# Kernel optimization log

Measured on AMD Instinct MI355X. Metric: run time of the kernel, lower is better.

The kernel has to match this reference:

```python
import jax, jax.numpy as jnp
import numpy as np

STAGE = 100  # number of weight bins


def _bin_reconstruct(w, affine):
    # Faithful vectorization of the 100-iter binning loop: element in bin i
    # (half-open interval) gets scaled by affine[i]; the max element falls
    # outside every bin (w < wmin + stage*range/stage fails) and is zeroed.
    flat = w.reshape(-1)
    wmin, wmax = flat.min(), flat.max()
    idx = jnp.floor((flat - wmin) / (wmax - wmin) * STAGE).astype(jnp.int32)
    mask = (idx < STAGE).astype(flat.dtype)  # mask is detached in torch (non-diff anyway)
    scale = affine[jnp.clip(idx, 0, STAGE - 1)]
    return flat * scale * mask


def _kl_vs_laplace(new_flat, lap):
    # F.kl_div(log_softmax(w), softmax(lap), reduction='none').mean()
    logq = jax.nn.log_softmax(new_flat)
    p = jax.nn.softmax(lap)
    return (p * (jnp.log(p) - logq)).mean()


def _adder2d(x, w, stride, padding, groups=1):
    # AdderNet conv: out = -sum_k |patch_k - w_k| (no bias)
    O, Cg, kh, kw = w.shape
    patches = jax.lax.conv_general_dilated_patches(
        x, (kh, kw), (stride, stride), [(padding, padding), (padding, padding)])
    B, _, Hp, Wp = patches.shape  # channel dim ordered (C, kh, kw), C-major
    if groups == 1:
        p = patches.reshape(B, 1, Cg * kh * kw, Hp, Wp)
        wf = w.reshape(1, O, Cg * kh * kw, 1, 1)
    else:  # depthwise: groups == C_in, Cg == 1, O == C_in
        p = patches.reshape(B, O, kh * kw, Hp, Wp)
        wf = w.reshape(1, O, kh * kw, 1, 1)
    return -jnp.abs(p - wf).sum(axis=2)  # [B, O, Hp, Wp]


def _bn_train(x, g, b, eps=1e-5):
    # BatchNorm2d in training mode (batch statistics, biased variance)
    m = x.mean(axis=(0, 2, 3), keepdims=True)
    v = ((x - m) ** 2).mean(axis=(0, 2, 3), keepdims=True)
    return (x - m) * jax.lax.rsqrt(v + eps) * g.reshape(1, -1, 1, 1) + b.reshape(1, -1, 1, 1)


def _forward(x, sw_ds, sw_c1, sw_c2, sw_c3, a_ds, a_c1, a_c2, a_c3, peg_w,
             g1, b1, g2, b2, g3, b3, gds, bds, lap_ds, lap_c1, lap_c2, lap_c3):
    kl = jnp.float32(0.0)
    f_ds = _bin_reconstruct(sw_ds, a_ds)
    kl = kl + _kl_vs_laplace(f_ds, lap_ds)
    f_c1 = _bin_reconstruct(sw_c1, a_c1)
    kl = kl + _kl_vs_laplace(f_c1, lap_c1)
    residual = jax.nn.relu(_bn_train(_adder2d(x, f_ds.reshape(sw_ds.shape), 1, 0), gds, bds))
    h = _adder2d(x, f_c1.reshape(sw_c1.shape), 1, 0)
    h = _adder2d(h, peg_w, 1, 1, groups=peg_w.shape[0])  # PEG depthwise 3x3
    h = jax.nn.relu(_bn_train(h, g1, b1))
    f_c2 = _bin_reconstruct(sw_c2, a_c2)
    kl = kl + _kl_vs_laplace(f_c2, lap_c2)
    h = _adder2d(h, f_c2.reshape(sw_c2.shape), 1, 1)
    h = jax.nn.relu(_bn_train(h, g2, b2))
    f_c3 = _bin_reconstruct(sw_c3, a_c3)
    kl = kl + _kl_vs_laplace(f_c3, lap_c3)
    h = _adder2d(h, f_c3.reshape(sw_c3.shape), 1, 0)
    h = _bn_train(h, g3, b3)  # bn3 gamma zero-initialized
    return jax.nn.relu(h + residual), kl


def setup_inputs() -> dict:
    key = jax.random.key(0)
    ks = jax.random.split(key, 16)
    inp = {
        'x': jax.random.normal(ks[0], (4, 128, 28, 28), jnp.float32),
        'sw_downsample': jax.random.normal(ks[1], (256, 128, 1, 1), jnp.float32) * 0.05,
        'sw_conv1': jax.random.normal(ks[2], (64, 128, 1, 1), jnp.float32) * 0.05,
        'sw_conv2': jax.random.normal(ks[3], (64, 64, 3, 3), jnp.float32) * 0.05,
        'sw_conv3': jax.random.normal(ks[4], (256, 64, 1, 1), jnp.float32) * 0.05,
        'downsample_affine': jax.random.normal(ks[5], (100,), jnp.float32),
        'conv1_affine': jax.random.normal(ks[6], (100,), jnp.float32),
        'conv2_affine': jax.random.normal(ks[7], (100,), jnp.float32),
        'conv3_affine': jax.random.normal(ks[8], (100,), jnp.float32),
        'peg_w': jax.random.normal(ks[9], (64, 1, 3, 3), jnp.float32) * 0.05,
        'bn1_g': jnp.ones((64,), jnp.float32), 'bn1_b': jnp.zeros((64,), jnp.float32),
        'bn2_g': jnp.ones((64,), jnp.float32), 'bn2_b': jnp.zeros((64,), jnp.float32),
        'bn3_g': jnp.zeros((256,), jnp.float32), 'bn3_b': jnp.zeros((256,), jnp.float32),
        'bnds_g': jnp.ones((256,), jnp.float32), 'bnds_b': jnp.zeros((256,), jnp.float32),
        # Laplace(0, 2) samples, drawn once in setup so the reference is deterministic
        'lap_ds': jax.random.laplace(ks[10], (32768,), jnp.float32) * 2.0,
        'lap_c1': jax.random.laplace(ks[11], (8192,), jnp.float32) * 2.0,
        'lap_c2': jax.random.laplace(ks[12], (36864,), jnp.float32) * 2.0,
        'lap_c3': jax.random.laplace(ks[13], (16384,), jnp.float32) * 2.0,
    }
    return inp


def reference(x, sw_downsample, sw_conv1, sw_conv2, sw_conv3,
              downsample_affine, conv1_affine, conv2_affine, conv3_affine, peg_w,
              bn1_g, bn1_b, bn2_g, bn2_b, bn3_g, bn3_b, bnds_g, bnds_b,
              lap_ds, lap_c1, lap_c2, lap_c3):
    return _forward(x, sw_downsample, sw_conv1, sw_conv2, sw_conv3,
                    downsample_affine, conv1_affine, conv2_affine, conv3_affine, peg_w,
                    bn1_g, bn1_b, bn2_g, bn2_b, bn3_g, bn3_b, bnds_g, bnds_b,
                    lap_ds, lap_c1, lap_c2, lap_c3)
```

## Files before the change

kernel.cpp:

```cpp
#include <hip/hip_runtime.h>
#include <math.h>


#define HW 784
#define NB 4
#define STAGE 100

__device__ __forceinline__ float wredSum(float v){
  for (int o = 32; o > 0; o >>= 1) v += __shfl_down(v, o, 64);
  return v;
}
__device__ __forceinline__ float wredMax(float v){
  for (int o = 32; o > 0; o >>= 1) v = fmaxf(v, __shfl_down(v, o, 64));
  return v;
}
__device__ __forceinline__ float wredMin(float v){
  for (int o = 32; o > 0; o >>= 1) v = fminf(v, __shfl_down(v, o, 64));
  return v;
}
__device__ __forceinline__ double wredSumD(double v){
  for (int o = 32; o > 0; o >>= 1) v += __shfl_down(v, o, 64);
  return v;
}

__device__ float blockMin4(float v){
  __shared__ float shn[4];
  __syncthreads();
  v = wredMin(v);
  if ((threadIdx.x & 63) == 0) shn[threadIdx.x >> 6] = v;
  __syncthreads();
  return fminf(fminf(shn[0], shn[1]), fminf(shn[2], shn[3]));
}
__device__ float blockMax4(float v){
  __shared__ float shx[4];
  __syncthreads();
  v = wredMax(v);
  if ((threadIdx.x & 63) == 0) shx[threadIdx.x >> 6] = v;
  __syncthreads();
  return fmaxf(fmaxf(shx[0], shx[1]), fmaxf(shx[2], shx[3]));
}

__device__ void stats4(float v0, float v1, float v2, float v3,
                       double* sumP, double* sqP, int oc0){
  __shared__ double sred[4][8];
  __syncthreads();
  const int w = threadIdx.x >> 6;
  float vv[4] = {v0, v1, v2, v3};
  #pragma unroll
  for (int i = 0; i < 4; i++){
    double d = (double)vv[i];
    double s = wredSumD(d);
    double q = wredSumD(d * d);
    if ((threadIdx.x & 63) == 0){ sred[w][i] = s; sred[w][4 + i] = q; }
  }
  __syncthreads();
  if (threadIdx.x < 8){
    double tot = sred[0][threadIdx.x] + sred[1][threadIdx.x]
               + sred[2][threadIdx.x] + sred[3][threadIdx.x];
    int i = threadIdx.x & 3;
    if (threadIdx.x < 4) atomicAdd(&sumP[oc0 + i], tot);
    else                 atomicAdd(&sqP[oc0 + i],  tot);
  }
}
__device__ void stats2(float v0, float v1, double* sumP, double* sqP, int oc0){
  __shared__ double sred2[4][4];
  __syncthreads();
  const int w = threadIdx.x >> 6;
  float vv[2] = {v0, v1};
  #pragma unroll
  for (int i = 0; i < 2; i++){
    double d = (double)vv[i];
    double s = wredSumD(d);
    double q = wredSumD(d * d);
    if ((threadIdx.x & 63) == 0){ sred2[w][i] = s; sred2[w][2 + i] = q; }
  }
  __syncthreads();
  if (threadIdx.x < 4){
    double tot = sred2[0][threadIdx.x] + sred2[1][threadIdx.x]
               + sred2[2][threadIdx.x] + sred2[3][threadIdx.x];
    int i = threadIdx.x & 1;
    if (threadIdx.x < 2) atomicAdd(&sumP[oc0 + i], tot);
    else                 atomicAdd(&sqP[oc0 + i],  tot);
  }
}

__device__ void klAccum(float se, float sel, float sef, float sq, double* dst){
  __shared__ double kls[4][4];
  __syncthreads();
  const int w = threadIdx.x >> 6;
  double a0 = wredSumD((double)se);
  double a1 = wredSumD((double)sel);
  double a2 = wredSumD((double)sef);
  double a3 = wredSumD((double)sq);
  if ((threadIdx.x & 63) == 0){
    kls[w][0] = a0; kls[w][1] = a1; kls[w][2] = a2; kls[w][3] = a3;
  }
  __syncthreads();
  if (threadIdx.x < 4){
    double tot = kls[0][threadIdx.x] + kls[1][threadIdx.x]
               + kls[2][threadIdx.x] + kls[3][threadIdx.x];
    atomicAdd(&dst[threadIdx.x], tot);
  }
}

__device__ __forceinline__ float reconv(float vv, float mn, float rng,
                                        const float* saff){
  float q = (vv - mn) / rng * 100.0f;
  int idx = (int)floorf(q);
  float nv = 0.0f;
  if (idx < STAGE){
    int ci = idx < 0 ? 0 : (idx > STAGE - 1 ? STAGE - 1 : idx);
    nv = vv * saff[ci];
  }
  return nv;
}

__device__ __forceinline__ void mmReduce(const float* mmbuf, int tens,
                                         float& mn, float& mx){
  mn = 3.402823466e38f; mx = -3.402823466e38f;
  #pragma unroll
  for (int k = 0; k < 16; k++){
    mn = fminf(mn, mmbuf[tens * 32 + k]);
    mx = fmaxf(mx, mmbuf[tens * 32 + 16 + k]);
  }
}

__global__ __launch_bounds__(256) void minmax_kernel(
    const float* w0, int n0, const float* w1, int n1,
    const float* w2, int n2, const float* w3, int n3,
    float* mmbuf, double* dstat)
{
  if (threadIdx.x < 21) dstat[blockIdx.x * 21 + threadIdx.x] = 0.0;
  const int tens = blockIdx.x >> 4, slot = blockIdx.x & 15;
  const float* w; int n;
  if      (tens == 0){ w = w0; n = n0; }
  else if (tens == 1){ w = w1; n = n1; }
  else if (tens == 2){ w = w2; n = n2; }
  else               { w = w3; n = n3; }
  float mn = 3.402823466e38f, mx = -3.402823466e38f;
  for (int i = slot * 256 + threadIdx.x; i < n; i += 4096){
    float v = w[i];
    mn = fminf(mn, v); mx = fmaxf(mx, v);
  }
  mn = blockMin4(mn); mx = blockMax4(mx);
  if (threadIdx.x == 0){
    mmbuf[tens * 32 + slot]      = mn;
    mmbuf[tens * 32 + 16 + slot] = mx;
  }
}

__global__ __launch_bounds__(256) void front_kernel(
    const float* __restrict__ x,
    const float* __restrict__ w_ds, const float* __restrict__ aff_ds,
    const float* __restrict__ lap_ds,
    const float* __restrict__ w_c1, const float* __restrict__ aff_c1,
    const float* __restrict__ lap_c1,
    const float* __restrict__ w_c2, const float* __restrict__ aff_c2,
    const float* __restrict__ lap_c2, float* __restrict__ f_c2,
    const float* __restrict__ w_c3, const float* __restrict__ aff_c3,
    const float* __restrict__ lap_c3,
    const float* __restrict__ peg_w, const float* __restrict__ mmbuf,
    float* __restrict__ A, float* __restrict__ T2, double* __restrict__ dS)
{
  const int t = threadIdx.x;
  if (blockIdx.x < 512){
    const int a = blockIdx.x;
    const int chunk = a & 3, og = (a >> 2) & 31, b = a >> 7;
    const int oc0 = og * 8;
    __shared__ float saff[STAGE];
    __shared__ float sw[1024];
    if (t < STAGE) saff[t] = aff_ds[t];
    float mn, mx; mmReduce(mmbuf, 0, mn, mx);
    const float rng = mx - mn;
    __syncthreads();
    for (int k = t; k < 1024; k += 256)
      sw[k] = reconv(w_ds[oc0 * 128 + k], mn, rng, saff);
    __syncthreads();

    const int px = chunk * 196 + t;
    float v0=0,v1=0,v2=0,v3=0,v4=0,v5=0,v6=0,v7=0;
    if (t < 196){
      const float* xp = x + (size_t)b * 128 * HW + px;
      float c0=0,c1=0,c2=0,c3=0,c4=0,c5=0,c6=0,c7=0;
      #pragma unroll 4
      for (int c = 0; c < 128; c++){
        float xv = xp[(size_t)c * HW];
        c0 += fabsf(xv - sw[c]);
        c1 += fabsf(xv - sw[128 + c]);
        c2 += fabsf(xv - sw[256 + c]);
        c3 += fabsf(xv - sw[384 + c]);
        c4 += fabsf(xv - sw[512 + c]);
        c5 += fabsf(xv - sw[640 + c]);
        c6 += fabsf(xv - sw[768 + c]);
        c7 += fabsf(xv - sw[896 + c]);
      }
      v0=-c0; v1=-c1; v2=-c2; v3=-c3; v4=-c4; v5=-c5; v6=-c6; v7=-c7;
      float* op = A + ((size_t)(b * 256 + oc0)) * HW + px;
      op[0]=v0; op[HW]=v1; op[2*HW]=v2; op[3*HW]=v3;
      op[4*HW]=v4; op[5*HW]=v5; op[6*HW]=v6; op[7*HW]=v7;
    }
    stats4(v0, v1, v2, v3, dS + 0, dS + 256, oc0);
    stats4(v4, v5, v6, v7, dS + 0, dS + 256, oc0 + 4);

    if (b == 0 && chunk == 0){
      float se = 0, sel = 0, sef = 0, sq = 0;
      for (int k = t; k < 1024; k += 256){
        float l = lap_ds[oc0 * 128 + k];
        float e = expf(l);
        se += e; sel += e * l; sef += e * sw[k];
        sq += expf(sw[k]);
      }
      klAccum(se, sel, sef, sq, dS + 1280 + 0);
    }
  } else if (blockIdx.x < 768){
    const int a = blockIdx.x - 512;
    const int rc = a & 3, og = (a >> 2) & 15, b = a >> 6;
    const int oc0 = og * 4;
    __shared__ float saffc[STAGE];
    __shared__ float swc[512];
    __shared__ float swp[36];
    __shared__ float sT1[4][256];
    if (t < STAGE) saffc[t] = aff_c1[t];
    if (t >= 128 && t < 164) swp[t - 128] = peg_w[oc0 * 9 + (t - 128)];
    float mn, mx; mmReduce(mmbuf, 1, mn, mx);
    const float rng = mx - mn;
    __syncthreads();
    for (int k = t; k < 512; k += 256)
      swc[k] = reconv(w_c1[oc0 * 128 + k], mn, rng, saffc);
    __syncthreads();

    if (t < 252){
      const int rr = t / 28;
      const int col = t - rr * 28;
      const int wr = rc * 7 - 1 + rr;
      float tv0 = 0, tv1 = 0, tv2 = 0, tv3 = 0;
      if (wr >= 0 && wr < 28){
        const float* xp = x + (size_t)b * 128 * HW + wr * 28 + col;
        float c0 = 0, c1 = 0, c2 = 0, c3 = 0;
        #pragma unroll 4
        for (int c = 0; c < 128; c++){
          float xv = xp[(size_t)c * HW];
          c0 += fabsf(xv - swc[c]);
          c1 += fabsf(xv - swc[128 + c]);
          c2 += fabsf(xv - swc[256 + c]);
          c3 += fabsf(xv - swc[384 + c]);
        }
        tv0 = -c0; tv1 = -c1; tv2 = -c2; tv3 = -c3;
      }
      sT1[0][t] = tv0; sT1[1][t] = tv1; sT1[2][t] = tv2; sT1[3][t] = tv3;
    }
    __syncthreads();
    float v0 = 0, v1 = 0, v2 = 0, v3 = 0;
    if (t < 196){
      const int r = t / 28, col = t - r * 28;
      float c0 = 0, c1 = 0, c2 = 0, c3 = 0;
      #pragma unroll
      for (int ky = 0; ky < 3; ky++){
        #pragma unroll
        for (int kx = 0; kx < 3; kx++){
          int cc = col + kx - 1;
          bool ok = (cc >= 0) && (cc < 28);
          int idx = ok ? ((r + ky) * 28 + cc) : 0;
          float p0 = ok ? sT1[0][idx] : 0.0f;
          float p1 = ok ? sT1[1][idx] : 0.0f;
          float p2 = ok ? sT1[2][idx] : 0.0f;
          float p3 = ok ? sT1[3][idx] : 0.0f;
          int wk = ky * 3 + kx;
          c0 += fabsf(p0 - swp[wk]);
          c1 += fabsf(p1 - swp[9 + wk]);
          c2 += fabsf(p2 - swp[18 + wk]);
          c3 += fabsf(p3 - swp[27 + wk]);
        }
      }
      v0 = -c0; v1 = -c1; v2 = -c2; v3 = -c3;
      const int opx = (rc * 7 + r) * 28 + col;
      float* op = T2 + ((size_t)(b * 64 + oc0)) * HW + opx;
      op[0] = v0; op[HW] = v1; op[2 * HW] = v2; op[3 * HW] = v3;
    }
    stats4(v0, v1, v2, v3, dS + 512, dS + 576, oc0);

    if (b == 0 && rc == 0){
      float se = 0, sel = 0, sef = 0, sq = 0;
      for (int k = t; k < 512; k += 256){
        float l = lap_c1[oc0 * 128 + k];
        float e = expf(l);
        se += e; sel += e * l; sef += e * swc[k];
        sq += expf(swc[k]);
      }
      klAccum(se, sel, sef, sq, dS + 1280 + 4);
    }
  } else if (blockIdx.x < 832){
    const int j = blockIdx.x - 768;
    __shared__ float saff2[STAGE];
    if (t < STAGE) saff2[t] = aff_c2[t];
    float mn, mx; mmReduce(mmbuf, 2, mn, mx);
    const float rng = mx - mn;
    __syncthreads();
    float se = 0, sel = 0, sef = 0, sq = 0;
    for (int k = t; k < 576; k += 256){
      float nv = reconv(w_c2[j * 576 + k], mn, rng, saff2);
      f_c2[j * 576 + k] = nv;
      float l = lap_c2[j * 576 + k];
      float e = expf(l);
      se += e; sel += e * l; sef += e * nv; sq += expf(nv);
    }
    klAccum(se, sel, sef, sq, dS + 1280 + 8);
  } else {
    const int j = blockIdx.x - 832;
    __shared__ float saff3[STAGE];
    if (t < STAGE) saff3[t] = aff_c3[t];
    float mn, mx; mmReduce(mmbuf, 3, mn, mx);
    const float rng = mx - mn;
    __syncthreads();
    float se = 0, sel = 0, sef = 0, sq = 0;
    for (int k = t; k < 1024; k += 256){
      float nv = reconv(w_c3[j * 1024 + k], mn, rng, saff3);
      float l = lap_c3[j * 1024 + k];
      float e = expf(l);
      se += e; sel += e * l; sef += e * nv; sq += expf(nv);
    }
    klAccum(se, sel, sef, sq, dS + 1280 + 12);
  }
}

__global__ __launch_bounds__(256) void bnapply_pad_kernel(
    const float* __restrict__ T2, float* __restrict__ T2b,
    const float* __restrict__ g1, const float* __restrict__ b1,
    const double* __restrict__ dS)
{
  const int a = blockIdx.x;
  const int c = a & 63, b = a >> 6;
  __shared__ float ssc, ssb;
  if (threadIdx.x == 0){
    double s  = dS[512 + c] * (1.0 / 3136.0);
    double vr = dS[576 + c] * (1.0 / 3136.0) - s * s;
    float scale = g1[c] * rsqrtf((float)vr + 1e-5f);
    ssc = scale; ssb = b1[c] - (float)s * scale;
  }
  __syncthreads();
  const float sc_ = ssc, bi_ = ssb;
  const float* src = T2 + (size_t)a * HW;
  float* dst = T2b + (size_t)a * 960;
  for (int i = threadIdx.x; i < 960; i += 256){
    int row = i >> 5, col = i & 31;
    float v = 0.0f;
    if (row >= 1 && row <= 28 && col >= 1 && col <= 28)
      v = fmaxf(src[(row - 1) * 28 + (col - 1)] * sc_ + bi_, 0.0f);
    dst[i] = v;
  }
}

__global__ __launch_bounds__(256) void mid3x3_kernel(
    const float* __restrict__ T2b, const float* __restrict__ f_c2,
    float* __restrict__ T3, double* __restrict__ dS)
{
  const int t = threadIdx.x;
  const int a = blockIdx.x;
  const int chunk = a & 3, og = (a >> 2) & 31, b = a >> 7;
  const int oc0 = og * 2;
  const float* __restrict__ wA = f_c2 + oc0 * 576;
  const float* __restrict__ wB = wA + 576;

  float v0 = 0, v1 = 0;
  const int px = chunk * 196 + t;
  if (t < 196){
    const int y = px / 28, xc = px - y * 28;
    const float* base = T2b + (size_t)b * 64 * 960 + y * 32 + xc;
    float c0 = 0, c1 = 0;
    #pragma unroll 2
    for (int c = 0; c < 64; c++){
      const float* p = base + c * 960;
      float t0 = p[0],  t1 = p[1],  t2 = p[2];
      float t3 = p[32], t4 = p[33], t5 = p[34];
      float t6 = p[64], t7 = p[65], t8 = p[66];
      const float* wa = wA + c * 9;
      const float* wb = wB + c * 9;
      c0 += fabsf(t0 - wa[0]) + fabsf(t1 - wa[1]) + fabsf(t2 - wa[2])
          + fabsf(t3 - wa[3]) + fabsf(t4 - wa[4]) + fabsf(t5 - wa[5])
          + fabsf(t6 - wa[6]) + fabsf(t7 - wa[7]) + fabsf(t8 - wa[8]);
      c1 += fabsf(t0 - wb[0]) + fabsf(t1 - wb[1]) + fabsf(t2 - wb[2])
          + fabsf(t3 - wb[3]) + fabsf(t4 - wb[4]) + fabsf(t5 - wb[5])
          + fabsf(t6 - wb[6]) + fabsf(t7 - wb[7]) + fabsf(t8 - wb[8]);
    }
    v0 = -c0; v1 = -c1;
    T3[((size_t)(b * 64 + oc0)) * HW + px]     = v0;
    T3[((size_t)(b * 64 + oc0 + 1)) * HW + px] = v1;
  }
  stats2(v0, v1, dS + 640, dS + 704, oc0);
}

__global__ __launch_bounds__(256) void back_kernel(
    const float* __restrict__ T3, const float* __restrict__ w_c3,
    const float* __restrict__ aff_c3, const float* __restrict__ mmbuf,
    const float* __restrict__ g2, const float* __restrict__ b2,
    float* __restrict__ out, double* __restrict__ dS)
{
  const int t = threadIdx.x;
  const int a = blockIdx.x;
  const int chunk = a & 3, og = (a >> 2) & 63, b = a >> 8;
  const int oc0 = og * 4;
  __shared__ float ssc[64], ssb[64], sw[256], saff[STAGE];
  if (t < 64){
    double s  = dS[640 + t] * (1.0 / 3136.0);
    double vr = dS[704 + t] * (1.0 / 3136.0) - s * s;
    float scale = g2[t] * rsqrtf((float)vr + 1e-5f);
    ssc[t] = scale; ssb[t] = b2[t] - (float)s * scale;
  }
  if (t >= 128 && t < 128 + STAGE) saff[t - 128] = aff_c3[t - 128];
  float mn, mx; mmReduce(mmbuf, 3, mn, mx);
  const float rng = mx - mn;
  __syncthreads();
  sw[t] = reconv(w_c3[oc0 * 64 + t], mn, rng, saff);
  __syncthreads();

  const int px = chunk * 196 + t;
  float v0 = 0, v1 = 0, v2 = 0, v3 = 0;
  if (t < 196){
    const float* bp = T3 + (size_t)b * 64 * HW + px;
    float c0 = 0, c1 = 0, c2 = 0, c3 = 0;
    #pragma unroll 4
    for (int c = 0; c < 64; c++){
      float raw = bp[(size_t)c * HW];
      float vv = fmaxf(raw * ssc[c] + ssb[c], 0.0f);
      c0 += fabsf(vv - sw[c]);
      c1 += fabsf(vv - sw[64 + c]);
      c2 += fabsf(vv - sw[128 + c]);
      c3 += fabsf(vv - sw[192 + c]);
    }
    v0 = -c0; v1 = -c1; v2 = -c2; v3 = -c3;
    float* op = out + ((size_t)(b * 256 + oc0)) * HW + px;
    op[0] = v0; op[HW] = v1; op[2 * HW] = v2; op[3 * HW] = v3;
  }
  stats4(v0, v1, v2, v3, dS + 768, dS + 1024, oc0);
}

__global__ __launch_bounds__(256) void final_kernel(
    float* __restrict__ out, const float* __restrict__ A,
    const float* __restrict__ g3, const float* __restrict__ b3,
    const float* __restrict__ gds, const float* __restrict__ bds,
    const double* __restrict__ dS)
{
  __shared__ float s3c[256], s3b[256], sdc[256], sdb[256];
  const int t = threadIdx.x;
  {
    double s  = dS[768 + t] * (1.0 / 3136.0);
    double vr = dS[1024 + t] * (1.0 / 3136.0) - s * s;
    float scale = g3[t] * rsqrtf((float)vr + 1e-5f);
    s3c[t] = scale; s3b[t] = b3[t] - (float)s * scale;
    s  = dS[t] * (1.0 / 3136.0);
    vr = dS[256 + t] * (1.0 / 3136.0) - s * s;
    scale = gds[t] * rsqrtf((float)vr + 1e-5f);
    sdc[t] = scale; sdb[t] = bds[t] - (float)s * scale;
  }
  __syncthreads();
  #pragma unroll
  for (int k = 0; k < 4; k++){
    int n = blockIdx.x * 1024 + k * 256 + t;
    int c = (n / HW) & 255;
    float h = out[n], aa = A[n];
    float r = fmaxf(aa * sdc[c] + sdb[c], 0.0f);
    out[n] = fmaxf(h * s3c[c] + s3b[c] + r, 0.0f);
  }
  if (blockIdx.x == 0 && t == 0){
    const int ns[4] = {32768, 8192, 36864, 16384};
    float kl = 0.0f;
    #pragma unroll
    for (int q = 0; q < 4; q++){
      double se  = dS[1280 + q * 4];
      double sel = dS[1280 + q * 4 + 1];
      double sef = dS[1280 + q * 4 + 2];
      double sq  = dS[1280 + q * 4 + 3];
      kl += (float)((((sel - sef) / se) - log(se) + log(sq)) / (double)ns[q]);
    }
    out[802816] = kl;
  }
}

extern "C" void kernel_launch(void* const* d_in, const int* in_sizes, int n_in,
                              void* d_out, int out_size, void* d_ws, size_t ws_size,
                              hipStream_t stream)
{
  const float* x      = (const float*)d_in[0];
  const float* sw_ds  = (const float*)d_in[1];
  const float* sw_c1  = (const float*)d_in[2];
  const float* sw_c2  = (const float*)d_in[3];
  const float* sw_c3  = (const float*)d_in[4];
  const float* a_ds   = (const float*)d_in[5];
  const float* a_c1   = (const float*)d_in[6];
  const float* a_c2   = (const float*)d_in[7];
  const float* a_c3   = (const float*)d_in[8];
  const float* peg_w  = (const float*)d_in[9];
  const float* bn1_g  = (const float*)d_in[10];
  const float* bn1_b  = (const float*)d_in[11];
  const float* bn2_g  = (const float*)d_in[12];
  const float* bn2_b  = (const float*)d_in[13];
  const float* bn3_g  = (const float*)d_in[14];
  const float* bn3_b  = (const float*)d_in[15];
  const float* bnds_g = (const float*)d_in[16];
  const float* bnds_b = (const float*)d_in[17];
  const float* lap_ds = (const float*)d_in[18];
  const float* lap_c1 = (const float*)d_in[19];
  const float* lap_c2 = (const float*)d_in[20];
  const float* lap_c3 = (const float*)d_in[21];

  float* ws    = (float*)d_ws;
  float* f_c2  = ws;
  float* mmbuf = ws + 36864;
  double* dstat= (double*)(ws + 37120);
  float* A     = ws + 39808;
  float* T2    = ws + 842624;
  float* T3    = ws + 1043328;
  float* T2b   = ws + 1244032;

  float* out = (float*)d_out;

  minmax_kernel<<<64, 256, 0, stream>>>(
      sw_ds, 32768, sw_c1, 8192, sw_c2, 36864, sw_c3, 16384, mmbuf, dstat);

  front_kernel<<<848, 256, 0, stream>>>(
      x, sw_ds, a_ds, lap_ds, sw_c1, a_c1, lap_c1,
      sw_c2, a_c2, lap_c2, f_c2, sw_c3, a_c3, lap_c3,
      peg_w, mmbuf, A, T2, dstat);

  bnapply_pad_kernel<<<256, 256, 0, stream>>>(T2, T2b, bn1_g, bn1_b, dstat);

  mid3x3_kernel<<<512, 256, 0, stream>>>(T2b, f_c2, T3, dstat);

  back_kernel<<<1024, 256, 0, stream>>>(T3, sw_c3, a_c3, mmbuf,
                                        bn2_g, bn2_b, out, dstat);

  final_kernel<<<784, 256, 0, stream>>>(out, A, bn3_g, bn3_b, bnds_g, bnds_b,
                                        dstat);
}
```

Baseline: 171.8 us.

## Fuse all stages into one persistent cooperative kernel with grid syncs

Replaces the six separate kernel launches with a single cooperative kernel of 512 blocks. Stages are separated by grid.sync(), and the work of each former kernel is remapped onto the fixed block count, with some blocks running two units. This removes per-launch overhead and inter-kernel gaps. In exchange it adds grid-wide barrier costs, imbalanced per-block work in the front stage, and a shared-memory footprint that is the union of every stage, which may limit occupancy.

```diff
diff --git a/kernel.cpp b/kernel.cpp
--- a/kernel.cpp
+++ b/kernel.cpp
@@ -1,15 +1,22 @@
 #include <hip/hip_runtime.h>
+#include <hip/hip_cooperative_groups.h>
 #include <math.h>
 
+
+namespace cg = cooperative_groups;
 
 #define HW 784
 #define NB 4
 #define STAGE 100
 
-__device__ __forceinline__ float wredSum(float v){
-  for (int o = 32; o > 0; o >>= 1) v += __shfl_down(v, o, 64);
-  return v;
-}
+struct Params {
+  const float *x, *w_ds, *a_ds, *lap_ds, *w_c1, *a_c1, *lap_c1;
+  const float *w_c2, *a_c2, *lap_c2, *w_c3, *a_c3, *lap_c3;
+  const float *peg_w, *g1, *b1, *g2, *b2, *g3, *b3, *gds, *bds;
+  float *f_c2, *mmbuf, *A, *T2, *T2b, *T3, *out;
+  double *dstat;
+};
+
 __device__ __forceinline__ float wredMax(float v){
   for (int o = 32; o > 0; o >>= 1) v = fmaxf(v, __shfl_down(v, o, 64));
   return v;
@@ -22,7 +29,6 @@
   for (int o = 32; o > 0; o >>= 1) v += __shfl_down(v, o, 64);
   return v;
 }
-
 __device__ float blockMin4(float v){
   __shared__ float shn[4];
   __syncthreads();
@@ -39,7 +45,6 @@
   __syncthreads();
   return fmaxf(fmaxf(shx[0], shx[1]), fmaxf(shx[2], shx[3]));
 }
-
 __device__ void stats4(float v0, float v1, float v2, float v3,
                        double* sumP, double* sqP, int oc0){
   __shared__ double sred[4][8];
@@ -83,7 +88,6 @@
     else                 atomicAdd(&sqP[oc0 + i],  tot);
   }
 }
-
 __device__ void klAccum(float se, float sel, float sef, float sq, double* dst){
   __shared__ double kls[4][4];
   __syncthreads();
@@ -102,7 +106,6 @@
     atomicAdd(&dst[threadIdx.x], tot);
   }
 }
-
 __device__ __forceinline__ float reconv(float vv, float mn, float rng,
                                         const float* saff){
   float q = (vv - mn) / rng * 100.0f;
@@ -114,7 +117,6 @@
   }
   return nv;
 }
-
 __device__ __forceinline__ void mmReduce(const float* mmbuf, int tens,
                                          float& mn, float& mx){
   mn = 3.402823466e38f; mx = -3.402823466e38f;
@@ -125,223 +127,190 @@
   }
 }
 
-__global__ __launch_bounds__(256) void minmax_kernel(
-    const float* w0, int n0, const float* w1, int n1,
-    const float* w2, int n2, const float* w3, int n3,
-    float* mmbuf, double* dstat)
-{
-  if (threadIdx.x < 21) dstat[blockIdx.x * 21 + threadIdx.x] = 0.0;
-  const int tens = blockIdx.x >> 4, slot = blockIdx.x & 15;
-  const float* w; int n;
-  if      (tens == 0){ w = w0; n = n0; }
-  else if (tens == 1){ w = w1; n = n1; }
-  else if (tens == 2){ w = w2; n = n2; }
-  else               { w = w3; n = n3; }
-  float mn = 3.402823466e38f, mx = -3.402823466e38f;
-  for (int i = slot * 256 + threadIdx.x; i < n; i += 4096){
-    float v = w[i];
-    mn = fminf(mn, v); mx = fmaxf(mx, v);
-  }
-  mn = blockMin4(mn); mx = blockMax4(mx);
-  if (threadIdx.x == 0){
-    mmbuf[tens * 32 + slot]      = mn;
-    mmbuf[tens * 32 + 16 + slot] = mx;
-  }
-}
-
-__global__ __launch_bounds__(256) void front_kernel(
-    const float* __restrict__ x,
-    const float* __restrict__ w_ds, const float* __restrict__ aff_ds,
-    const float* __restrict__ lap_ds,
-    const float* __restrict__ w_c1, const float* __restrict__ aff_c1,
-    const float* __restrict__ lap_c1,
-    const float* __restrict__ w_c2, const float* __restrict__ aff_c2,
-    const float* __restrict__ lap_c2, float* __restrict__ f_c2,
-    const float* __restrict__ w_c3, const float* __restrict__ aff_c3,
-    const float* __restrict__ lap_c3,
-    const float* __restrict__ peg_w, const float* __restrict__ mmbuf,
-    float* __restrict__ A, float* __restrict__ T2, double* __restrict__ dS)
-{
+__device__ void dsUnit(int u, const Params& p){
   const int t = threadIdx.x;
-  if (blockIdx.x < 512){
-    const int a = blockIdx.x;
-    const int chunk = a & 3, og = (a >> 2) & 31, b = a >> 7;
-    const int oc0 = og * 8;
-    __shared__ float saff[STAGE];
-    __shared__ float sw[1024];
-    if (t < STAGE) saff[t] = aff_ds[t];
-    float mn, mx; mmReduce(mmbuf, 0, mn, mx);
-    const float rng = mx - mn;
-    __syncthreads();
-    for (int k = t; k < 1024; k += 256)
-      sw[k] = reconv(w_ds[oc0 * 128 + k], mn, rng, saff);
-    __syncthreads();
-
-    const int px = chunk * 196 + t;
-    float v0=0,v1=0,v2=0,v3=0,v4=0,v5=0,v6=0,v7=0;
-    if (t < 196){
-      const float* xp = x + (size_t)b * 128 * HW + px;
-      float c0=0,c1=0,c2=0,c3=0,c4=0,c5=0,c6=0,c7=0;
+  const int chunk = u & 3, og = (u >> 2) & 31, b = u >> 7;
+  const int oc0 = og * 8;
+  __shared__ float ds_saff[STAGE];
+  __shared__ float ds_sw[1024];
+  __syncthreads();
+  if (t < STAGE) ds_saff[t] = p.a_ds[t];
+  float mn, mx; mmReduce(p.mmbuf, 0, mn, mx);
+  const float rng = mx - mn;
+  __syncthreads();
+  for (int k = t; k < 1024; k += 256)
+    ds_sw[k] = reconv(p.w_ds[oc0 * 128 + k], mn, rng, ds_saff);
+  __syncthreads();
+
+  const int px = chunk * 196 + t;
+  float v0=0,v1=0,v2=0,v3=0,v4=0,v5=0,v6=0,v7=0;
+  if (t < 196){
+    const float* xp = p.x + (size_t)b * 128 * HW + px;
+    float c0=0,c1=0,c2=0,c3=0,c4=0,c5=0,c6=0,c7=0;
+    #pragma unroll 4
+    for (int c = 0; c < 128; c++){
+      float xv = xp[(size_t)c * HW];
+      c0 += fabsf(xv - ds_sw[c]);
+      c1 += fabsf(xv - ds_sw[128 + c]);
+      c2 += fabsf(xv - ds_sw[256 + c]);
+      c3 += fabsf(xv - ds_sw[384 + c]);
+      c4 += fabsf(xv - ds_sw[512 + c]);
+      c5 += fabsf(xv - ds_sw[640 + c]);
+      c6 += fabsf(xv - ds_sw[768 + c]);
+      c7 += fabsf(xv - ds_sw[896 + c]);
+    }
+    v0=-c0; v1=-c1; v2=-c2; v3=-c3; v4=-c4; v5=-c5; v6=-c6; v7=-c7;
+    float* op = p.A + ((size_t)(b * 256 + oc0)) * HW + px;
+    op[0]=v0; op[HW]=v1; op[2*HW]=v2; op[3*HW]=v3;
+    op[4*HW]=v4; op[5*HW]=v5; op[6*HW]=v6; op[7*HW]=v7;
+  }
+  stats4(v0, v1, v2, v3, p.dstat + 0, p.dstat + 256, oc0);
+  stats4(v4, v5, v6, v7, p.dstat + 0, p.dstat + 256, oc0 + 4);
+
+  if (chunk == 0 && b == 0){
+    float se = 0, sel = 0, sef = 0, sq = 0;
+    for (int k = t; k < 1024; k += 256){
+      float l = p.lap_ds[oc0 * 128 + k];
+      float e = expf(l);
+      se += e; sel += e * l; sef += e * ds_sw[k];
+      sq += expf(ds_sw[k]);
+    }
+    klAccum(se, sel, sef, sq, p.dstat + 1280 + 0);
+  }
+}
+
+__device__ void c1Unit(int a, const Params& p){
+  const int t = threadIdx.x;
+  const int rc = a & 3, og = (a >> 2) & 15, b = a >> 6;
+  const int oc0 = og * 4;
+  __shared__ float c1_saff[STAGE];
+  __shared__ float c1_swc[512];
+  __shared__ float c1_swp[36];
+  __shared__ float c1_sT1[4][256];
+  if (t < STAGE) c1_saff[t] = p.a_c1[t];
+  if (t >= 128 && t < 164) c1_swp[t - 128] = p.peg_w[oc0 * 9 + (t - 128)];
+  float mn, mx; mmReduce(p.mmbuf, 1, mn, mx);
+  const float rng = mx - mn;
+  __syncthreads();
+  for (int k = t; k < 512; k += 256)
+    c1_swc[k] = reconv(p.w_c1[oc0 * 128 + k], mn, rng, c1_saff);
+  __syncthreads();
+
+  if (t < 252){
+    const int rr = t / 28;
+    const int col = t - rr * 28;
+    const int wr = rc * 7 - 1 + rr;
+    float tv0 = 0, tv1 = 0, tv2 = 0, tv3 = 0;
+    if (wr >= 0 && wr < 28){
+      const float* xp = p.x + (size_t)b * 128 * HW + wr * 28 + col;
+      float c0 = 0, c1 = 0, c2 = 0, c3 = 0;
       #pragma unroll 4
       for (int c = 0; c < 128; c++){
         float xv = xp[(size_t)c * HW];
-        c0 += fabsf(xv - sw[c]);
-        c1 += fabsf(xv - sw[128 + c]);
-        c2 += fabsf(xv - sw[256 + c]);
-        c3 += fabsf(xv - sw[384 + c]);
-        c4 += fabsf(xv - sw[512 + c]);
-        c5 += fabsf(xv - sw[640 + c]);
-        c6 += fabsf(xv - sw[768 + c]);
-        c7 += fabsf(xv - sw[896 + c]);
+        c0 += fabsf(xv - c1_swc[c]);
+        c1 += fabsf(xv - c1_swc[128 + c]);
+        c2 += fabsf(xv - c1_swc[256 + c]);
+        c3 += fabsf(xv - c1_swc[384 + c]);
       }
-      v0=-c0; v1=-c1; v2=-c2; v3=-c3; v4=-c4; v5=-c5; v6=-c6; v7=-c7;
-      float* op = A + ((size_t)(b * 256 + oc0)) * HW + px;
-      op[0]=v0; op[HW]=v1; op[2*HW]=v2; op[3*HW]=v3;
-      op[4*HW]=v4; op[5*HW]=v5; op[6*HW]=v6; op[7*HW]=v7;
-    }
-    stats4(v0, v1, v2, v3, dS + 0, dS + 256, oc0);
-    stats4(v4, v5, v6, v7, dS + 0, dS + 256, oc0 + 4);
-
-    if (b == 0 && chunk == 0){
-      float se = 0, sel = 0, sef = 0, sq = 0;
-      for (int k = t; k < 1024; k += 256){
-        float l = lap_ds[oc0 * 128 + k];
-        float e = expf(l);
-        se += e; sel += e * l; sef += e * sw[k];
-        sq += expf(sw[k]);
+      tv0 = -c0; tv1 = -c1; tv2 = -c2; tv3 = -c3;
+    }
+    c1_sT1[0][t] = tv0; c1_sT1[1][t] = tv1;
+    c1_sT1[2][t] = tv2; c1_sT1[3][t] = tv3;
+  }
+  __syncthreads();
+  float v0 = 0, v1 = 0, v2 = 0, v3 = 0;
+  if (t < 196){
+    const int r = t / 28, col = t - r * 28;
+    float c0 = 0, c1 = 0, c2 = 0, c3 = 0;
+    #pragma unroll
+    for (int ky = 0; ky < 3; ky++){
+      #pragma unroll
+      for (int kx = 0; kx < 3; kx++){
+        int cc = col + kx - 1;
+        bool ok = (cc >= 0) && (cc < 28);
+        int idx = ok ? ((r + ky) * 28 + cc) : 0;
+        float p0 = ok ? c1_sT1[0][idx] : 0.0f;
+        float p1 = ok ? c1_sT1[1][idx] : 0.0f;
+        float p2 = ok ? c1_sT1[2][idx] : 0.0f;
+        float p3 = ok ? c1_sT1[3][idx] : 0.0f;
+        int wk = ky * 3 + kx;
+        c0 += fabsf(p0 - c1_swp[wk]);
+        c1 += fabsf(p1 - c1_swp[9 + wk]);
+        c2 += fabsf(p2 - c1_swp[18 + wk]);
+        c3 += fabsf(p3 - c1_swp[27 + wk]);
       }
-      klAccum(se, sel, sef, sq, dS + 1280 + 0);
-    }
-  } else if (blockIdx.x < 768){
-    const int a = blockIdx.x - 512;
-    const int rc = a & 3, og = (a >> 2) & 15, b = a >> 6;
-    const int oc0 = og * 4;
-    __shared__ float saffc[STAGE];
-    __shared__ float swc[512];
-    __shared__ float swp[36];
-    __shared__ float sT1[4][256];
-    if (t < STAGE) saffc[t] = aff_c1[t];
-    if (t >= 128 && t < 164) swp[t - 128] = peg_w[oc0 * 9 + (t - 128)];
-    float mn, mx; mmReduce(mmbuf, 1, mn, mx);
-    const float rng = mx - mn;
-    __syncthreads();
-    for (int k = t; k < 512; k += 256)
-      swc[k] = reconv(w_c1[oc0 * 128 + k], mn, rng, saffc);
-    __syncthreads();
-
-    if (t < 252){
-      const int rr = t / 28;
-      const int col = t - rr * 28;
-      const int wr = rc * 7 - 1 + rr;
-      float tv0 = 0, tv1 = 0, tv2 = 0, tv3 = 0;
-      if (wr >= 0 && wr < 28){
-        const float* xp = x + (size_t)b * 128 * HW + wr * 28 + col;
-        float c0 = 0, c1 = 0, c2 = 0, c3 = 0;
-        #pragma unroll 4
-        for (int c = 0; c < 128; c++){
-          float xv = xp[(size_t)c * HW];
-          c0 += fabsf(xv - swc[c]);
-          c1 += fabsf(xv - swc[128 + c]);
-          c2 += fabsf(xv - swc[256 + c]);
-          c3 += fabsf(xv - swc[384 + c]);
-        }
-        tv0 = -c0; tv1 = -c1; tv2 = -c2; tv3 = -c3;
-      }
-      sT1[0][t] = tv0; sT1[1][t] = tv1; sT1[2][t] = tv2; sT1[3][t] = tv3;
-    }
-    __syncthreads();
-    float v0 = 0, v1 = 0, v2 = 0, v3 = 0;
-    if (t < 196){
-      const int r = t / 28, col = t - r * 28;
-      float c0 = 0, c1 = 0, c2 = 0, c3 = 0;
-      #pragma unroll
-      for (int ky = 0; ky < 3; ky++){
-        #pragma unroll
-        for (int kx = 0; kx < 3; kx++){
-          int cc = col + kx - 1;
-          bool ok = (cc >= 0) && (cc < 28);
-          int idx = ok ? ((r + ky) * 28 + cc) : 0;
-          float p0 = ok ? sT1[0][idx] : 0.0f;
-          float p1 = ok ? sT1[1][idx] : 0.0f;
-          float p2 = ok ? sT1[2][idx] : 0.0f;
-          float p3 = ok ? sT1[3][idx] : 0.0f;
-          int wk = ky * 3 + kx;
-          c0 += fabsf(p0 - swp[wk]);
-          c1 += fabsf(p1 - swp[9 + wk]);
-          c2 += fabsf(p2 - swp[18 + wk]);
-          c3 += fabsf(p3 - swp[27 + wk]);
-        }
-      }
-      v0 = -c0; v1 = -c1; v2 = -c2; v3 = -c3;
-      const int opx = (rc * 7 + r) * 28 + col;
-      float* op = T2 + ((size_t)(b * 64 + oc0)) * HW + opx;
-      op[0] = v0; op[HW] = v1; op[2 * HW] = v2; op[3 * HW] = v3;
-    }
-    stats4(v0, v1, v2, v3, dS + 512, dS + 576, oc0);
-
-    if (b == 0 && rc == 0){
-      float se = 0, sel = 0, sef = 0, sq = 0;
-      for (int k = t; k < 512; k += 256){
-        float l = lap_c1[oc0 * 128 + k];
-        float e = expf(l);
-        se += e; sel += e * l; sef += e * swc[k];
-        sq += expf(swc[k]);
-      }
-      klAccum(se, sel, sef, sq, dS + 1280 + 4);
-    }
-  } else if (blockIdx.x < 832){
-    const int j = blockIdx.x - 768;
-    __shared__ float saff2[STAGE];
-    if (t < STAGE) saff2[t] = aff_c2[t];
-    float mn, mx; mmReduce(mmbuf, 2, mn, mx);
-    const float rng = mx - mn;
-    __syncthreads();
+    }
+    v0 = -c0; v1 = -c1; v2 = -c2; v3 = -c3;
+    const int opx = (rc * 7 + r) * 28 + col;
+    float* op = p.T2 + ((size_t)(b * 64 + oc0)) * HW + opx;
+    op[0] = v0; op[HW] = v1; op[2 * HW] = v2; op[3 * HW] = v3;
+  }
+  stats4(v0, v1, v2, v3, p.dstat + 512, p.dstat + 576, oc0);
+
+  if (b == 0 && rc == 0){
     float se = 0, sel = 0, sef = 0, sq = 0;
-    for (int k = t; k < 576; k += 256){
-      float nv = reconv(w_c2[j * 576 + k], mn, rng, saff2);
-      f_c2[j * 576 + k] = nv;
-      float l = lap_c2[j * 576 + k];
+    for (int k = t; k < 512; k += 256){
+      float f = c1_swc[k];
+      float l = p.lap_c1[oc0 * 128 + k];
       float e = expf(l);
-      se += e; sel += e * l; sef += e * nv; sq += expf(nv);
-    }
-    klAccum(se, sel, sef, sq, dS + 1280 + 8);
-  } else {
-    const int j = blockIdx.x - 832;
-    __shared__ float saff3[STAGE];
-    if (t < STAGE) saff3[t] = aff_c3[t];
-    float mn, mx; mmReduce(mmbuf, 3, mn, mx);
-    const float rng = mx - mn;
-    __syncthreads();
-    float se = 0, sel = 0, sef = 0, sq = 0;
-    for (int k = t; k < 1024; k += 256){
-      float nv = reconv(w_c3[j * 1024 + k], mn, rng, saff3);
-      float l = lap_c3[j * 1024 + k];
-      float e = expf(l);
-      se += e; sel += e * l; sef += e * nv; sq += expf(nv);
-    }
-    klAccum(se, sel, sef, sq, dS + 1280 + 12);
-  }
-}
-
-__global__ __launch_bounds__(256) void bnapply_pad_kernel(
-    const float* __restrict__ T2, float* __restrict__ T2b,
-    const float* __restrict__ g1, const float* __restrict__ b1,
-    const double* __restrict__ dS)
-{
-  const int a = blockIdx.x;
-  const int c = a & 63, b = a >> 6;
-  __shared__ float ssc, ssb;
+      se += e; sel += e * l; sef += e * f; sq += expf(f);
+    }
+    klAccum(se, sel, sef, sq, p.dstat + 1280 + 4);
+  }
+}
+
+__device__ void fc2Unit(int j, const Params& p){
+  const int t = threadIdx.x;
+  __shared__ float f2_saff[STAGE];
+  __syncthreads();
+  if (t < STAGE) f2_saff[t] = p.a_c2[t];
+  float mn, mx; mmReduce(p.mmbuf, 2, mn, mx);
+  const float rng = mx - mn;
+  __syncthreads();
+  float se = 0, sel = 0, sef = 0, sq = 0;
+  for (int k = t; k < 576; k += 256){
+    float nv = reconv(p.w_c2[j * 576 + k], mn, rng, f2_saff);
+    p.f_c2[j * 576 + k] = nv;
+    float l = p.lap_c2[j * 576 + k];
+    float e = expf(l);
+    se += e; sel += e * l; sef += e * nv; sq += expf(nv);
+  }
+  klAccum(se, sel, sef, sq, p.dstat + 1280 + 8);
+}
+__device__ void klt3Unit(int j, const Params& p){
+  const int t = threadIdx.x;
+  __shared__ float t3_saff[STAGE];
+  __syncthreads();
+  if (t < STAGE) t3_saff[t] = p.a_c3[t];
+  float mn, mx; mmReduce(p.mmbuf, 3, mn, mx);
+  const float rng = mx - mn;
+  __syncthreads();
+  float se = 0, sel = 0, sef = 0, sq = 0;
+  for (int k = t; k < 1024; k += 256){
+    float nv = reconv(p.w_c3[j * 1024 + k], mn, rng, t3_saff);
+    float l = p.lap_c3[j * 1024 + k];
+    float e = expf(l);
+    se += e; sel += e * l; sef += e * nv; sq += expf(nv);
+  }
+  klAccum(se, sel, sef, sq, p.dstat + 1280 + 12);
+}
+
+__device__ void bnpadHalf(int u, const Params& p){
+  const int a = u >> 1, half = u & 1;
+  const int c = a & 63;
+  __shared__ float bp_sc, bp_sb;
+  __syncthreads();
   if (threadIdx.x == 0){
-    double s  = dS[512 + c] * (1.0 / 3136.0);
-    double vr = dS[576 + c] * (1.0 / 3136.0) - s * s;
-    float scale = g1[c] * rsqrtf((float)vr + 1e-5f);
-    ssc = scale; ssb = b1[c] - (float)s * scale;
-  }
-  __syncthreads();
-  const float sc_ = ssc, bi_ = ssb;
-  const float* src = T2 + (size_t)a * HW;
-  float* dst = T2b + (size_t)a * 960;
-  for (int i = threadIdx.x; i < 960; i += 256){
+    double s  = p.dstat[512 + c] * (1.0 / 3136.0);
+    double vr = p.dstat[576 + c] * (1.0 / 3136.0) - s * s;
+    float scale = p.g1[c] * rsqrtf((float)vr + 1e-5f);
+    bp_sc = scale; bp_sb = p.b1[c] - (float)s * scale;
+  }
+  __syncthreads();
+  const float sc_ = bp_sc, bi_ = bp_sb;
+  const float* src = p.T2 + (size_t)a * HW;
+  float* dst = p.T2b + (size_t)a * 960;
+  for (int i = half * 480 + threadIdx.x; i < half * 480 + 480; i += 256){
     int row = i >> 5, col = i & 31;
     float v = 0.0f;
     if (row >= 1 && row <= 28 && col >= 1 && col <= 28)
@@ -350,29 +319,25 @@
   }
 }
 
-__global__ __launch_bounds__(256) void mid3x3_kernel(
-    const float* __restrict__ T2b, const float* __restrict__ f_c2,
-    float* __restrict__ T3, double* __restrict__ dS)
-{
+__device__ void midUnit(int u, const Params& p){
   const int t = threadIdx.x;
-  const int a = blockIdx.x;
-  const int chunk = a & 3, og = (a >> 2) & 31, b = a >> 7;
+  const int chunk = u & 3, og = (u >> 2) & 31, b = u >> 7;
   const int oc0 = og * 2;
-  const float* __restrict__ wA = f_c2 + oc0 * 576;
-  const float* __restrict__ wB = wA + 576;
+  const float* wA = p.f_c2 + oc0 * 576;
+  const float* wB = wA + 576;
 
   float v0 = 0, v1 = 0;
   const int px = chunk * 196 + t;
   if (t < 196){
     const int y = px / 28, xc = px - y * 28;
-    const float* base = T2b + (size_t)b * 64 * 960 + y * 32 + xc;
+    const float* base = p.T2b + (size_t)b * 64 * 960 + y * 32 + xc;
     float c0 = 0, c1 = 0;
     #pragma unroll 2
     for (int c = 0; c < 64; c++){
-      const float* p = base + c * 960;
-      float t0 = p[0],  t1 = p[1],  t2 = p[2];
-      float t3 = p[32], t4 = p[33], t5 = p[34];
-      float t6 = p[64], t7 = p[65], t8 = p[66];
+      const float* pp = base + c * 960;
+      float t0 = pp[0],  t1 = pp[1],  t2 = pp[2];
+      float t3 = pp[32], t4 = pp[33], t5 = pp[34];
+      float t6 = pp[64], t7 = pp[65], t8 = pp[66];
       const float* wa = wA + c * 9;
       const float* wb = wB + c * 9;
       c0 += fabsf(t0 - wa[0]) + fabsf(t1 - wa[1]) + fabsf(t2 - wa[2])
@@ -383,96 +348,136 @@
           + fabsf(t6 - wb[6]) + fabsf(t7 - wb[7]) + fabsf(t8 - wb[8]);
     }
     v0 = -c0; v1 = -c1;
-    T3[((size_t)(b * 64 + oc0)) * HW + px]     = v0;
-    T3[((size_t)(b * 64 + oc0 + 1)) * HW + px] = v1;
-  }
-  stats2(v0, v1, dS + 640, dS + 704, oc0);
-}
-
-__global__ __launch_bounds__(256) void back_kernel(
-    const float* __restrict__ T3, const float* __restrict__ w_c3,
-    const float* __restrict__ aff_c3, const float* __restrict__ mmbuf,
-    const float* __restrict__ g2, const float* __restrict__ b2,
-    float* __restrict__ out, double* __restrict__ dS)
-{
+    p.T3[((size_t)(b * 64 + oc0)) * HW + px]     = v0;
+    p.T3[((size_t)(b * 64 + oc0 + 1)) * HW + px] = v1;
+  }
+  stats2(v0, v1, p.dstat + 640, p.dstat + 704, oc0);
+}
+
+__device__ void backUnit(int u, const Params& p){
   const int t = threadIdx.x;
-  const int a = blockIdx.x;
-  const int chunk = a & 3, og = (a >> 2) & 63, b = a >> 8;
+  const int chunk = u & 3, og = (u >> 2) & 63, b = u >> 8;
   const int oc0 = og * 4;
-  __shared__ float ssc[64], ssb[64], sw[256], saff[STAGE];
+  __shared__ float bk_sc[64], bk_sb[64], bk_sw[256], bk_saff[STAGE];
+  __syncthreads();
   if (t < 64){
-    double s  = dS[640 + t] * (1.0 / 3136.0);
-    double vr = dS[704 + t] * (1.0 / 3136.0) - s * s;
-    float scale = g2[t] * rsqrtf((float)vr + 1e-5f);
-    ssc[t] = scale; ssb[t] = b2[t] - (float)s * scale;
-  }
-  if (t >= 128 && t < 128 + STAGE) saff[t - 128] = aff_c3[t - 128];
-  float mn, mx; mmReduce(mmbuf, 3, mn, mx);
+    double s  = p.dstat[640 + t] * (1.0 / 3136.0);
+    double vr = p.dstat[704 + t] * (1.0 / 3136.0) - s * s;
+    float scale = p.g2[t] * rsqrtf((float)vr + 1e-5f);
+    bk_sc[t] = scale; bk_sb[t] = p.b2[t] - (float)s * scale;
+  }
+  if (t >= 128 && t < 128 + STAGE) bk_saff[t - 128] = p.a_c3[t - 128];
+  float mn, mx; mmReduce(p.mmbuf, 3, mn, mx);
   const float rng = mx - mn;
   __syncthreads();
-  sw[t] = reconv(w_c3[oc0 * 64 + t], mn, rng, saff);
+  bk_sw[t] = reconv(p.w_c3[oc0 * 64 + t], mn, rng, bk_saff);
   __syncthreads();
 
   const int px = chunk * 196 + t;
   float v0 = 0, v1 = 0, v2 = 0, v3 = 0;
   if (t < 196){
-    const float* bp = T3 + (size_t)b * 64 * HW + px;
+    const float* bp = p.T3 + (size_t)b * 64 * HW + px;
     float c0 = 0, c1 = 0, c2 = 0, c3 = 0;
     #pragma unroll 4
     for (int c = 0; c < 64; c++){
       float raw = bp[(size_t)c * HW];
-      float vv = fmaxf(raw * ssc[c] + ssb[c], 0.0f);
-      c0 += fabsf(vv - sw[c]);
-      c1 += fabsf(vv - sw[64 + c]);
-      c2 += fabsf(vv - sw[128 + c]);
-      c3 += fabsf(vv - sw[192 + c]);
+      float vv = fmaxf(raw * bk_sc[c] + bk_sb[c], 0.0f);
+      c0 += fabsf(vv - bk_sw[c]);
+      c1 += fabsf(vv - bk_sw[64 + c]);
+      c2 += fabsf(vv - bk_sw[128 + c]);
+      c3 += fabsf(vv - bk_sw[192 + c]);
     }
     v0 = -c0; v1 = -c1; v2 = -c2; v3 = -c3;
-    float* op = out + ((size_t)(b * 256 + oc0)) * HW + px;
+    float* op = p.out + ((size_t)(b * 256 + oc0)) * HW + px;
     op[0] = v0; op[HW] = v1; op[2 * HW] = v2; op[3 * HW] = v3;
   }
-  stats4(v0, v1, v2, v3, dS + 768, dS + 1024, oc0);
-}
-
-__global__ __launch_bounds__(256) void final_kernel(
-    float* __restrict__ out, const float* __restrict__ A,
-    const float* __restrict__ g3, const float* __restrict__ b3,
-    const float* __restrict__ gds, const float* __restrict__ bds,
-    const double* __restrict__ dS)
-{
+  stats4(v0, v1, v2, v3, p.dstat + 768, p.dstat + 1024, oc0);
+}
+
+__global__ __launch_bounds__(256) void fused_kernel(Params p){
+  cg::grid_group grid = cg::this_grid();
+  const int blk = blockIdx.x, t = threadIdx.x;
+
+  if (t < 3 && blk * 3 + t < 1296) p.dstat[blk * 3 + t] = 0.0;
+  if (blk < 64){
+    const int tens = blk >> 4, slot = blk & 15;
+    const float* w; int n;
+    if      (tens == 0){ w = p.w_ds; n = 32768; }
+    else if (tens == 1){ w = p.w_c1; n = 8192; }
+    else if (tens == 2){ w = p.w_c2; n = 36864; }
+    else               { w = p.w_c3; n = 16384; }
+    float mn = 3.402823466e38f, mx = -3.402823466e38f;
+    for (int i = slot * 256 + t; i < n; i += 4096){
+      float v = w[i];
+      mn = fminf(mn, v); mx = fmaxf(mx, v);
+    }
+    mn = blockMin4(mn); mx = blockMax4(mx);
+    if (t == 0){
+      p.mmbuf[tens * 32 + slot]      = mn;
+      p.mmbuf[tens * 32 + 16 + slot] = mx;
+    }
+  }
+  grid.sync();
+
+  if (blk < 256){
+    c1Unit(blk, p);
+    dsUnit(blk, p);
+  } else {
+    dsUnit(blk, p);
+    int r = blk - 256;
+    if (r < 64) fc2Unit(r, p);
+    else if (r < 80) klt3Unit(r - 64, p);
+  }
+  grid.sync();
+
+  bnpadHalf(blk, p);
+  grid.sync();
+
+  midUnit(blk, p);
+  grid.sync();
+
+  backUnit(blk, p);
+  backUnit(blk + 512, p);
+  grid.sync();
+
   __shared__ float s3c[256], s3b[256], sdc[256], sdb[256];
-  const int t = threadIdx.x;
+  __syncthreads();
   {
-    double s  = dS[768 + t] * (1.0 / 3136.0);
-    double vr = dS[1024 + t] * (1.0 / 3136.0) - s * s;
-    float scale = g3[t] * rsqrtf((float)vr + 1e-5f);
-    s3c[t] = scale; s3b[t] = b3[t] - (float)s * scale;
-    s  = dS[t] * (1.0 / 3136.0);
-    vr = dS[256 + t] * (1.0 / 3136.0) - s * s;
-    scale = gds[t] * rsqrtf((float)vr + 1e-5f);
-    sdc[t] = scale; sdb[t] = bds[t] - (float)s * scale;
-  }
-  __syncthreads();
-  #pragma unroll
-  for (int k = 0; k < 4; k++){
-    int n = blockIdx.x * 1024 + k * 256 + t;
-    int c = (n / HW) & 255;
-    float h = out[n], aa = A[n];
-    float r = fmaxf(aa * sdc[c] + sdb[c], 0.0f);
-    out[n] = fmaxf(h * s3c[c] + s3b[c] + r, 0.0f);
-  }
-  if (blockIdx.x == 0 && t == 0){
+    double s  = p.dstat[768 + t] * (1.0 / 3136.0);
+    double vr = p.dstat[1024 + t] * (1.0 / 3136.0) - s * s;
+    float scale = p.g3[t] * rsqrtf((float)vr + 1e-5f);
+    s3c[t] = scale; s3b[t] = p.b3[t] - (float)s * scale;
+    s  = p.dstat[t] * (1.0 / 3136.0);
+    vr = p.dstat[256 + t] * (1.0 / 3136.0) - s * s;
+    scale = p.gds[t] * rsqrtf((float)vr + 1e-5f);
+    sdc[t] = scale; sdb[t] = p.bds[t] - (float)s * scale;
+  }
+  __syncthreads();
+  for (int rep = 0; rep < 2; rep++){
+    int u = blk + rep * 512;
+    if (u < 784){
+      #pragma unroll
+      for (int k = 0; k < 4; k++){
+        int n = u * 1024 + k * 256 + t;
+        int c = (n / HW) & 255;
+        float h = p.out[n], aa = p.A[n];
+        float r = fmaxf(aa * sdc[c] + sdb[c], 0.0f);
+        p.out[n] = fmaxf(h * s3c[c] + s3b[c] + r, 0.0f);
+      }
+    }
+  }
+  if (blk == 0 && t == 0){
     const int ns[4] = {32768, 8192, 36864, 16384};
     float kl = 0.0f;
     #pragma unroll
     for (int q = 0; q < 4; q++){
-      double se  = dS[1280 + q * 4];
-      double sel = dS[1280 + q * 4 + 1];
-      double sef = dS[1280 + q * 4 + 2];
-      double sq  = dS[1280 + q * 4 + 3];
+      double se  = p.dstat[1280 + q * 4];
+      double sel = p.dstat[1280 + q * 4 + 1];
+      double sef = p.dstat[1280 + q * 4 + 2];
+      double sq  = p.dstat[1280 + q * 4 + 3];
       kl += (float)((((sel - sef) / se) - log(se) + log(sq)) / (double)ns[q]);
     }
-    out[802816] = kl;
+    p.out[802816] = kl;
   }
 }
 
@@ -480,55 +485,42 @@
                               void* d_out, int out_size, void* d_ws, size_t ws_size,
                               hipStream_t stream)
 {
-  const float* x      = (const float*)d_in[0];
-  const float* sw_ds  = (const float*)d_in[1];
-  const float* sw_c1  = (const float*)d_in[2];
-  const float* sw_c2  = (const float*)d_in[3];
-  const float* sw_c3  = (const float*)d_in[4];
-  const float* a_ds   = (const float*)d_in[5];
-  const float* a_c1   = (const float*)d_in[6];
-  const float* a_c2   = (const float*)d_in[7];
-  const float* a_c3   = (const float*)d_in[8];
-  const float* peg_w  = (const float*)d_in[9];
-  const float* bn1_g  = (const float*)d_in[10];
-  const float* bn1_b  = (const float*)d_in[11];
-  const float* bn2_g  = (const float*)d_in[12];
-  const float* bn2_b  = (const float*)d_in[13];
-  const float* bn3_g  = (const float*)d_in[14];
-  const float* bn3_b  = (const float*)d_in[15];
-  const float* bnds_g = (const float*)d_in[16];
-  const float* bnds_b = (const float*)d_in[17];
-  const float* lap_ds = (const float*)d_in[18];
-  const float* lap_c1 = (const float*)d_in[19];
-  const float* lap_c2 = (const float*)d_in[20];
-  const float* lap_c3 = (const float*)d_in[21];
-
-  float* ws    = (float*)d_ws;
-  float* f_c2  = ws;
-  float* mmbuf = ws + 36864;
-  double* dstat= (double*)(ws + 37120);
-  float* A     = ws + 39808;
-  float* T2    = ws + 842624;
-  float* T3    = ws + 1043328;
-  float* T2b   = ws + 1244032;
-
-  float* out = (float*)d_out;
-
-  minmax_kernel<<<64, 256, 0, stream>>>(
-      sw_ds, 32768, sw_c1, 8192, sw_c2, 36864, sw_c3, 16384, mmbuf, dstat);
-
-  front_kernel<<<848, 256, 0, stream>>>(
-      x, sw_ds, a_ds, lap_ds, sw_c1, a_c1, lap_c1,
-      sw_c2, a_c2, lap_c2, f_c2, sw_c3, a_c3, lap_c3,
-      peg_w, mmbuf, A, T2, dstat);
-
-  bnapply_pad_kernel<<<256, 256, 0, stream>>>(T2, T2b, bn1_g, bn1_b, dstat);
-
-  mid3x3_kernel<<<512, 256, 0, stream>>>(T2b, f_c2, T3, dstat);
-
-  back_kernel<<<1024, 256, 0, stream>>>(T3, sw_c3, a_c3, mmbuf,
-                                        bn2_g, bn2_b, out, dstat);
-
-  final_kernel<<<784, 256, 0, stream>>>(out, A, bn3_g, bn3_b, bnds_g, bnds_b,
-                                        dstat);
-}
+  float* ws = (float*)d_ws;
+
+  Params p;
+  p.x      = (const float*)d_in[0];
+  p.w_ds   = (const float*)d_in[1];
+  p.w_c1   = (const float*)d_in[2];
+  p.w_c2   = (const float*)d_in[3];
+  p.w_c3   = (const float*)d_in[4];
+  p.a_ds   = (const float*)d_in[5];
+  p.a_c1   = (const float*)d_in[6];
+  p.a_c2   = (const float*)d_in[7];
+  p.a_c3   = (const float*)d_in[8];
+  p.peg_w  = (const float*)d_in[9];
+  p.g1     = (const float*)d_in[10];
+  p.b1     = (const float*)d_in[11];
+  p.g2     = (const float*)d_in[12];
+  p.b2     = (const float*)d_in[13];
+  p.g3     = (const float*)d_in[14];
+  p.b3     = (const float*)d_in[15];
+  p.gds    = (const float*)d_in[16];
+  p.bds    = (const float*)d_in[17];
+  p.lap_ds = (const float*)d_in[18];
+  p.lap_c1 = (const float*)d_in[19];
+  p.lap_c2 = (const float*)d_in[20];
+  p.lap_c3 = (const float*)d_in[21];
+
+  p.f_c2  = ws;
+  p.mmbuf = ws + 36864;
+  p.dstat = (double*)(ws + 36992);
+  p.A     = ws + 39680;
+  p.T2    = ws + 842496;
+  p.T3    = ws + 1043200;
+  p.T2b   = ws + 1243904;
+  p.out   = (float*)d_out;
+
+  void* args[] = { &p };
+  hipLaunchCooperativeKernel(reinterpret_cast<void*>(fused_kernel),
+                             dim3(512), dim3(256), args, 0, stream);
+}
```

Result: slower. 464.7 us (+170.4%).
